# Optimization experiments

Measured on AMD Instinct MI355X. Metric: run time of the kernel, lower is better.

The kernel has to match this reference:

```python
import jax, jax.numpy as jnp
import numpy as np

N_HEAD = 16

def setup_inputs() -> dict:
    key = jax.random.key(0)
    ks = jax.random.split(key, 5)
    B, T, C = 8, 1024, 1024
    s = 0.02
    return {
        "x": jax.random.normal(ks[0], (B, T, C), jnp.float32),
        "W_qkv": jax.random.normal(ks[1], (C, 3 * C), jnp.float32) * s,
        "b_qkv": jnp.zeros((3 * C,), jnp.float32),
        "W_proj": jax.random.normal(ks[2], (C, C), jnp.float32) * s,
        "b_proj": jnp.zeros((C,), jnp.float32),
    }

def reference(x, W_qkv, b_qkv, W_proj, b_proj):
    B, T, C = x.shape
    H = N_HEAD
    hs = C // H
    qkv = x @ W_qkv + b_qkv                       # [B,T,3C]
    q, k, v = jnp.split(qkv, 3, axis=-1)
    # [B,T,C] -> [B,H,T,hs]
    q = q.reshape(B, T, H, hs).transpose(0, 2, 1, 3)
    k = k.reshape(B, T, H, hs).transpose(0, 2, 1, 3)
    v = v.reshape(B, T, H, hs).transpose(0, 2, 1, 3)
    scores = jnp.einsum('bhqd,bhkd->bhqk', q, k) * (hs ** -0.5)  # [B,H,T,T]
    causal = jnp.tril(jnp.ones((T, T), dtype=bool))
    scores = jnp.where(causal[None, None], scores, jnp.finfo(scores.dtype).min)
    attn = jax.nn.softmax(scores, axis=-1)
    # dropout layers are identity in eval mode
    out = jnp.einsum('bhqk,bhkd->bhqd', attn, v)  # [B,H,T,hs]
    out = out.transpose(0, 2, 1, 3).reshape(B, T, C)
    return out @ W_proj + b_proj
```

## Files before the change

kernel.cpp:

```cpp
#include <hip/hip_runtime.h>

#define TT 1024
#define CC 1024
#define NH 16
#define HS 64

typedef __attribute__((ext_vector_type(8))) short short8;
typedef __attribute__((ext_vector_type(4))) float f32x4;

__device__ inline unsigned short f2bf(float f) {
  unsigned int u = __float_as_uint(f);
  unsigned int r = u + 0x7FFFu + ((u >> 16) & 1u);
  return (unsigned short)(r >> 16);
}

__device__ inline unsigned int cvtpk_bf16(float lo, float hi) {
  unsigned int r;
  asm("v_cvt_pk_bf16_f32 %0, %1, %2" : "=v"(r) : "v"(lo), "v"(hi));
  return r;
}

#define GLDS16(g, l)                                                         \
  __builtin_amdgcn_global_load_lds(                                          \
      (const __attribute__((address_space(1))) void*)(g),                    \
      (__attribute__((address_space(3))) void*)(l), 16, 0, 0)

__global__ __launch_bounds__(256) void f32_to_bf16(
    const float* __restrict__ in, unsigned short* __restrict__ out, int n4) {
  int i = (blockIdx.x * 256 + threadIdx.x);
  if (i >= n4) return;
  float4 v = *(const float4*)&in[(size_t)i * 4];
  ushort4 o;
  o.x = f2bf(v.x); o.y = f2bf(v.y); o.z = f2bf(v.z); o.w = f2bf(v.w);
  *(ushort4*)&out[(size_t)i * 4] = o;
}

__global__ __launch_bounds__(256) void transpose_to_bf16(
    const float* __restrict__ W, unsigned short* __restrict__ Wt,
    int K, int N) {
  __shared__ float tile[32][33];
  const int n0 = blockIdx.x * 32, k0 = blockIdx.y * 32;
  const int t = threadIdx.x;
  {
    const int kr = t >> 3;
    const int nc = (t & 7) * 4;
    float4 v = *(const float4*)&W[(size_t)(k0 + kr) * N + n0 + nc];
    tile[kr][nc + 0] = v.x; tile[kr][nc + 1] = v.y;
    tile[kr][nc + 2] = v.z; tile[kr][nc + 3] = v.w;
  }
  __syncthreads();
  {
    const int nr = t >> 3;
    const int kc = (t & 7) * 4;
    ushort4 o;
    o.x = f2bf(tile[kc + 0][nr]);
    o.y = f2bf(tile[kc + 1][nr]);
    o.z = f2bf(tile[kc + 2][nr]);
    o.w = f2bf(tile[kc + 3][nr]);
    *(ushort4*)&Wt[(size_t)(n0 + nr) * K + k0 + kc] = o;
  }
}

template <bool BF16_OUT>
__global__ __launch_bounds__(512, 2) void gemm_8ph(
    const unsigned short* __restrict__ A,
    const unsigned short* __restrict__ Bt,
    const float* __restrict__ bias,
    void* __restrict__ Cv,
    int M, int N, int K) {
  extern __shared__ __attribute__((aligned(16))) unsigned short smg[];
  typedef __attribute__((address_space(3))) unsigned short lds_us;
  lds_us* sml = (lds_us*)smg;

  const int tid = threadIdx.x;
  const int w = tid >> 6, l = tid & 63;
  const int lr = l & 15, lg = l >> 4;
  const int wm = w >> 2, wn = w & 3;

  const int gx = gridDim.x;
  const int nwg = gx * gridDim.y;
  int f = blockIdx.y * gx + blockIdx.x;
  f = (f & 7) * (nwg >> 3) + (f >> 3);
  const int bx = f % gx, by = f / gx;
  const int brow = by * 256, bcol = bx * 256;

  const int r0 = w * 8 + (l >> 3);
  const int cs = (l & 7) ^ (l >> 3);
  const unsigned short* Asrc = A + (size_t)(brow + r0) * K + cs * 8;
  const unsigned short* Bsrc = Bt + (size_t)(bcol + r0) * K + cs * 8;
  const int wlds = w * 512;

#define ST_A(dd, hh, qq, kt)                                                 \
  GLDS16(Asrc + (size_t)((hh)*128 + (qq)*64) * K + (kt) * 64,                \
         sml + (dd)*16384 + (hh)*8192 + (qq)*4096 + wlds)
#define ST_B(dd, hh, qq, kt)                                                 \
  GLDS16(Bsrc + (size_t)((hh)*128 + (qq)*64) * K + (kt) * 64,                \
         sml + 32768 + (dd)*16384 + (hh)*8192 + (qq)*4096 + wlds)

  f32x4 acc[8][4] = {};
  short8 afA[4][2], bfB[4][2];

  const int ck0 = ((lg) ^ (lr & 7)) * 8;
  const int ck1 = ((4 | lg) ^ (lr & 7)) * 8;
  const int abase = wm * 8192 + lr * 64;
  const int bbase = 32768 + (wn >> 1) * 8192 + (wn & 1) * 4096 + lr * 64;

#define LDA(MI0)                                                             \
  _Pragma("unroll") for (int mi = 0; mi < 4; ++mi) {                         \
    afA[mi][0] = *(const short8*)(smg + bb * 16384 + abase + ((MI0) + mi) * 1024 + ck0); \
    afA[mi][1] = *(const short8*)(smg + bb * 16384 + abase + ((MI0) + mi) * 1024 + ck1); \
  }
#define LDB(NI0)                                                             \
  _Pragma("unroll") for (int ni = 0; ni < 2; ++ni) {                         \
    bfB[(NI0) + ni][0] = *(const short8*)(smg + bb * 16384 + bbase + ((NI0) + ni) * 1024 + ck0); \
    bfB[(NI0) + ni][1] = *(const short8*)(smg + bb * 16384 + bbase + ((NI0) + ni) * 1024 + ck1); \
  }
#define MFMA_Q(MI0, NI0)                                                     \
  __builtin_amdgcn_s_setprio(1);                                             \
  _Pragma("unroll") for (int mi = 0; mi < 4; ++mi)                           \
  _Pragma("unroll") for (int ni = 0; ni < 2; ++ni)                           \
  _Pragma("unroll") for (int ks = 0; ks < 2; ++ks)                           \
    acc[(MI0) + mi][(NI0) + ni] = __builtin_amdgcn_mfma_f32_16x16x32_bf16(   \
        afA[mi][ks], bfB[(NI0) + ni][ks], acc[(MI0) + mi][(NI0) + ni], 0, 0, 0); \
  __builtin_amdgcn_s_setprio(0);
#define WAIT_LGKM                                                            \
  asm volatile("s_waitcnt lgkmcnt(0)" ::: "memory");                         \
  __builtin_amdgcn_sched_barrier(0);

  const int nk = K >> 6;

#pragma unroll
  for (int tt = 0; tt < 2; ++tt) {
    ST_A(tt, 0, 0, tt); ST_A(tt, 0, 1, tt); ST_A(tt, 1, 0, tt); ST_A(tt, 1, 1, tt);
    ST_B(tt, 0, 0, tt); ST_B(tt, 0, 1, tt); ST_B(tt, 1, 0, tt); ST_B(tt, 1, 1, tt);
  }

  for (int t = 0; t < nk; ++t) {
    const int bb = t & 1;
    const bool dostage = (t + 2 < nk);
    if (t == nk - 1) { asm volatile("s_waitcnt vmcnt(0)" ::: "memory"); }
    else             { asm volatile("s_waitcnt vmcnt(8)" ::: "memory"); }
    __builtin_amdgcn_sched_barrier(0);
    __builtin_amdgcn_s_barrier();
    LDA(0); LDB(0);
    WAIT_LGKM;
    MFMA_Q(0, 0);
    __builtin_amdgcn_s_barrier();
    LDB(2);
    WAIT_LGKM;
    MFMA_Q(0, 2);
    __builtin_amdgcn_s_barrier();
    if (dostage) { ST_B(bb, 0, 0, t + 2); ST_B(bb, 0, 1, t + 2);
                   ST_B(bb, 1, 0, t + 2); ST_B(bb, 1, 1, t + 2); }
    LDA(4);
    WAIT_LGKM;
    MFMA_Q(4, 0);
    __builtin_amdgcn_s_barrier();
    if (dostage) { ST_A(bb, 0, 0, t + 2); ST_A(bb, 0, 1, t + 2);
                   ST_A(bb, 1, 0, t + 2); ST_A(bb, 1, 1, t + 2); }
    MFMA_Q(4, 2);
    __builtin_amdgcn_s_barrier();
  }
#undef ST_A
#undef ST_B
#undef LDA
#undef LDB
#undef MFMA_Q
#undef WAIT_LGKM

#pragma unroll
  for (int ni = 0; ni < 4; ++ni) {
    const int col = bcol + wn * 64 + ni * 16 + lr;
    const float bv = bias[col];
#pragma unroll
    for (int mi = 0; mi < 8; ++mi) {
      const int row0 = brow + wm * 128 + mi * 16 + lg * 4;
#pragma unroll
      for (int j = 0; j < 4; ++j) {
        const float val = acc[mi][ni][j] + bv;
        if (BF16_OUT)
          ((unsigned short*)Cv)[(size_t)(row0 + j) * N + col] = f2bf(val);
        else
          ((float*)Cv)[(size_t)(row0 + j) * N + col] = val;
      }
    }
  }
}

template <bool BF16_OUT>
__global__ __launch_bounds__(512, 4) void gemm_bt_256(
    const unsigned short* __restrict__ A,
    const unsigned short* __restrict__ Bt,
    const float* __restrict__ bias,
    void* __restrict__ Cv,
    int M, int N, int K) {
  __shared__ __attribute__((aligned(16))) unsigned short As[2][256 * 32];
  __shared__ __attribute__((aligned(16))) unsigned short Bs[2][128 * 32];

  const int tid = threadIdx.x;
  const int w = tid >> 6, l = tid & 63;
  const int lr = l & 15, lg = l >> 4;
  const int wr = w >> 1, wc = w & 1;

  const int gx = gridDim.x;
  const int nwg = gx * gridDim.y;
  int f = blockIdx.y * gx + blockIdx.x;
  f = (f & 7) * (nwg >> 3) + (f >> 3);
  const int bx = f % gx, by = f / gx;
  const int brow = by * 256, bcol = bx * 128;

  const int ga0 = tid, ga1 = 512 + tid;
  const int ar0 = ga0 >> 2, ac0 = ga0 & 3;
  const int ar1 = ga1 >> 2, ac1 = ga1 & 3;
  const int br_ = tid >> 2, bc_ = tid & 3;
  const unsigned short* Asrc0 =
      A + (size_t)(brow + ar0) * K + (ac0 ^ ((ar0 >> 1) & 3)) * 8;
  const unsigned short* Asrc1 =
      A + (size_t)(brow + ar1) * K + (ac1 ^ ((ar1 >> 1) & 3)) * 8;
  const unsigned short* Bsrc =
      Bt + (size_t)(bcol + br_) * K + (bc_ ^ ((br_ >> 1) & 3)) * 8;

  typedef __attribute__((address_space(3))) unsigned short lds_us;

#define STAGE(bb, kt)                                                        \
  do {                                                                       \
    const int k0_ = (kt) * 32;                                               \
    GLDS16(Asrc0 + k0_, (lds_us*)&As[bb][0] + ga0 * 8);                      \
    GLDS16(Asrc1 + k0_, (lds_us*)&As[bb][0] + ga1 * 8);                      \
    GLDS16(Bsrc + k0_, (lds_us*)&Bs[bb][0] + tid * 8);                       \
  } while (0)

  f32x4 acc[4][4] = {};

  const int sfr = ((((lr >> 1) & 3) ^ lg) * 8);
  const int arow0 = wr * 64 + lr;
  const int brow0 = wc * 64 + lr;

#define KSTEP(cur, kt, VMASM, DOSTAGE)                                       \
  do {                                                                       \
    asm volatile(VMASM ::: "memory");                                        \
    __builtin_amdgcn_sched_barrier(0);                                       \
    __builtin_amdgcn_s_barrier();                                            \
    short8 af[4], bf[4];                                                     \
    _Pragma("unroll") for (int mi_ = 0; mi_ < 4; ++mi_)                      \
        af[mi_] = *(const short8*)&As[cur][(arow0 + mi_ * 16) * 32 + sfr];   \
    _Pragma("unroll") for (int ni_ = 0; ni_ < 4; ++ni_)                      \
        bf[ni_] = *(const short8*)&Bs[cur][(brow0 + ni_ * 16) * 32 + sfr];   \
    asm volatile("s_waitcnt lgkmcnt(0)" ::: "memory");                       \
    __builtin_amdgcn_sched_barrier(0);                                       \
    __builtin_amdgcn_s_barrier();                                            \
    __builtin_amdgcn_sched_barrier(0);                                       \
    if (DOSTAGE) STAGE(cur, (kt) + 2);                                       \
    __builtin_amdgcn_s_setprio(1);                                           \
    _Pragma("unroll") for (int mi_ = 0; mi_ < 4; ++mi_)                      \
        _Pragma("unroll") for (int ni_ = 0; ni_ < 4; ++ni_)                  \
            acc[mi_][ni_] = __builtin_amdgcn_mfma_f32_16x16x32_bf16(         \
                af[mi_], bf[ni_], acc[mi_][ni_], 0, 0, 0);                   \
    __builtin_amdgcn_s_setprio(0);                                           \
  } while (0)

  const int nk = K >> 5;
  STAGE(0, 0);
  STAGE(1, 1);
  int cur = 0;
  for (int t = 0; t < nk - 1; ++t) {
    KSTEP(cur, t, "s_waitcnt vmcnt(3)", (t + 2 < nk));
    cur ^= 1;
  }
  KSTEP(cur, nk - 1, "s_waitcnt vmcnt(0)", false);
#undef KSTEP
#undef STAGE

#pragma unroll
  for (int ni = 0; ni < 4; ++ni) {
    const int col = bcol + wc * 64 + ni * 16 + lr;
    const float bv = bias[col];
#pragma unroll
    for (int mi = 0; mi < 4; ++mi) {
      const int row0 = brow + wr * 64 + mi * 16 + lg * 4;
#pragma unroll
      for (int j = 0; j < 4; ++j) {
        const float val = acc[mi][ni][j] + bv;
        if (BF16_OUT)
          ((unsigned short*)Cv)[(size_t)(row0 + j) * N + col] = f2bf(val);
        else
          ((float*)Cv)[(size_t)(row0 + j) * N + col] = val;
      }
    }
  }
}

#define C1 0.18033688f

__global__ __launch_bounds__(256) void attn_mfma(
    const unsigned short* __restrict__ qkv, unsigned short* __restrict__ aout) {
  const int bh = blockIdx.y;
  const int b = bh >> 4, h = bh & 15;
  const int tid = threadIdx.x;
  const int w = tid >> 6;
  const int l = tid & 63;
  const int lr = l & 15;
  const int lg = l >> 4;

  __shared__ __attribute__((aligned(16))) unsigned short Kl[64 * 64];
  __shared__ __attribute__((aligned(16))) unsigned short Vt[64 * 64];
  __shared__ __attribute__((aligned(16))) unsigned short Pq[4][32 * 64];

  const size_t row3c = 3 * CC;
  const unsigned short* qbase = qkv + (size_t)(b * TT) * row3c + h * HS;
  const unsigned short* kbase = qbase + CC;
  const unsigned short* vbase = qbase + 2 * CC;

  const int ksrow = 16 * w + (l >> 3);
  const int ksbyte = (((l & 7) ^ (l >> 3)) << 4);
  typedef __attribute__((address_space(3))) unsigned short lds_us;
  lds_us* KlW0 = (lds_us*)Kl + (16 * w) * 64;
  lds_us* KlW1 = (lds_us*)Kl + (16 * w + 8) * 64;

#pragma unroll 1
  for (int pass = 0; pass < 2; ++pass) {
    const int qt = pass ? (7 - blockIdx.x) : blockIdx.x;
    const int qw = qt * 128 + w * 32;

    short8 aq[2][2];
#pragma unroll
    for (int mi = 0; mi < 2; ++mi)
#pragma unroll
      for (int ks = 0; ks < 2; ++ks)
        aq[mi][ks] = *(const short8*)(qbase +
            (size_t)(qw + mi * 16 + lr) * row3c + ks * 32 + lg * 8);

    f32x4 sOT[4][2] = {};
    float lpart[2] = {0.f, 0.f};

    const int ntiles = 2 * qt + 2;
    for (int kt = 0; kt < ntiles; ++kt) {
      const int k0 = kt * 64;
      GLDS16((const char*)(kbase + (size_t)(k0 + ksrow) * row3c) + ksbyte, KlW0);
      GLDS16((const char*)(kbase + (size_t)(k0 + 8 + ksrow) * row3c) + ksbyte, KlW1);
      {
        const unsigned short* vsrc = vbase + (size_t)(k0 + l) * row3c + 16 * w;
        short8 v0 = *(const short8*)(vsrc);
        short8 v1 = *(const short8*)(vsrc + 8);
#pragma unroll
        for (int i = 0; i < 8; ++i) {
          const int d0 = 16 * w + i, d1 = d0 + 8;
          Vt[(d0 * 64 + l) ^ ((d0 & 7) << 3)] = (unsigned short)v0[i];
          Vt[(d1 * 64 + l) ^ ((d1 & 7) << 3)] = (unsigned short)v1[i];
        }
      }
      __syncthreads();

      if (k0 <= qw + 31) {
        f32x4 sacc[4][2] = {};
        short8 ak[4][2];
#pragma unroll
        for (int ni = 0; ni < 4; ++ni) {
          const int tok = ni * 16 + lr;
          const int sw = (tok & 7) << 3;
#pragma unroll
          for (int ks = 0; ks < 2; ++ks)
            ak[ni][ks] = *(const short8*)&Kl[tok * 64 + ((ks * 32 + lg * 8) ^ sw)];
        }
#pragma unroll
        for (int ni = 0; ni < 4; ++ni)
#pragma unroll
          for (int mi = 0; mi < 2; ++mi)
#pragma unroll
            for (int ks = 0; ks < 2; ++ks)
              sacc[ni][mi] = __builtin_amdgcn_mfma_f32_16x16x32_bf16(
                  ak[ni][ks], aq[mi][ks], sacc[ni][mi], 0, 0, 0);

        const bool diag = (k0 + 63 > qw);
#pragma unroll
        for (int mi = 0; mi < 2; ++mi) {
          const int qloc = mi * 16 + lr;
          const int qglob = qw + qloc;
          const int psw = (qloc & 7) << 3;
          float ls = 0.f;
#pragma unroll
          for (int ni = 0; ni < 4; ++ni) {
            float p[4];
#pragma unroll
            for (int jj = 0; jj < 4; ++jj) {
              const float pv = exp2f(fmaf(sacc[ni][mi][jj], C1, -2.0f));
              const int kvg = k0 + ni * 16 + lg * 4 + jj;
              p[jj] = (diag && (kvg > qglob)) ? 0.f : pv;
            }
            ls += (p[0] + p[1]) + (p[2] + p[3]);
            uint2 pk;
            pk.x = cvtpk_bf16(p[0], p[1]);
            pk.y = cvtpk_bf16(p[2], p[3]);
            *(uint2*)&Pq[w][qloc * 64 + ((ni * 16 + lg * 4) ^ psw)] = pk;
          }
          lpart[mi] += ls;
        }

        short8 av[4][2], bp[2][2];
#pragma unroll
        for (int nd = 0; nd < 4; ++nd) {
          const int d = nd * 16 + lr;
          const int sw = (d & 7) << 3;
#pragma unroll
          for (int ks = 0; ks < 2; ++ks)
            av[nd][ks] = *(const short8*)&Vt[d * 64 + ((ks * 32 + lg * 8) ^ sw)];
        }
#pragma unroll
        for (int mi = 0; mi < 2; ++mi) {
          const int qloc = mi * 16 + lr;
          const int psw = (qloc & 7) << 3;
#pragma unroll
          for (int ks = 0; ks < 2; ++ks)
            bp[mi][ks] = *(const short8*)&Pq[w][qloc * 64 + ((ks * 32 + lg * 8) ^ psw)];
        }
#pragma unroll
        for (int nd = 0; nd < 4; ++nd)
#pragma unroll
          for (int mi = 0; mi < 2; ++mi)
#pragma unroll
            for (int ks = 0; ks < 2; ++ks)
              sOT[nd][mi] = __builtin_amdgcn_mfma_f32_16x16x32_bf16(
                  av[nd][ks], bp[mi][ks], sOT[nd][mi], 0, 0, 0);
      }
      __syncthreads();
    }

#pragma unroll
    for (int mi = 0; mi < 2; ++mi) {
      float ls = lpart[mi];
      ls += __shfl_xor(ls, 16);
      ls += __shfl_xor(ls, 32);
      const float inv = 1.f / ls;
      const size_t row = (size_t)(b * TT + qw + mi * 16 + lr);
#pragma unroll
      for (int nd = 0; nd < 4; ++nd) {
        uint2 pk;
        pk.x = cvtpk_bf16(sOT[nd][mi][0] * inv, sOT[nd][mi][1] * inv);
        pk.y = cvtpk_bf16(sOT[nd][mi][2] * inv, sOT[nd][mi][3] * inv);
        *(uint2*)&aout[row * CC + h * HS + nd * 16 + lg * 4] = pk;
      }
    }
  }
}

extern "C" void kernel_launch(void* const* d_in, const int* in_sizes, int n_in,
                              void* d_out, int out_size, void* d_ws, size_t ws_size,
                              hipStream_t stream) {
  const float* x     = (const float*)d_in[0];
  const float* Wqkv  = (const float*)d_in[1];
  const float* bqkv  = (const float*)d_in[2];
  const float* Wproj = (const float*)d_in[3];
  const float* bproj = (const float*)d_in[4];
  float* out = (float*)d_out;

  char* ws = (char*)d_ws;
  unsigned short* qkvb   = (unsigned short*)ws;
  unsigned short* xb     = (unsigned short*)(ws + 50331648);
  unsigned short* attnb  = (unsigned short*)(ws + 67108864);
  unsigned short* wqkvt  = (unsigned short*)(ws + 83886080);
  unsigned short* wprojt = (unsigned short*)(ws + 90177536);

  const int M = 8 * TT;

  (void)hipFuncSetAttribute((const void*)&gemm_8ph<true>,
      hipFuncAttributeMaxDynamicSharedMemorySize, 131072);

  f32_to_bf16<<<dim3(8192), dim3(256), 0, stream>>>(x, xb, M * CC / 4);
  transpose_to_bf16<<<dim3(96, 32), dim3(256), 0, stream>>>(Wqkv, wqkvt, CC, 3 * CC);
  transpose_to_bf16<<<dim3(32, 32), dim3(256), 0, stream>>>(Wproj, wprojt, CC, CC);

  gemm_8ph<true><<<dim3(3 * CC / 256, M / 256), dim3(512), 131072, stream>>>(
      xb, wqkvt, bqkv, qkvb, M, 3 * CC, CC);

  attn_mfma<<<dim3(4, 8 * NH), dim3(256), 0, stream>>>(qkvb, attnb);

  gemm_bt_256<false><<<dim3(CC / 128, M / 256), dim3(512), 0, stream>>>(
      attnb, wprojt, bproj, out, M, CC, CC);
}
```

Baseline: 251.7 us.

## Restagger A/B global-to-LDS prefetch across GEMM k-loop phases

Reworks the double-buffered GEMM main loop so A tiles for step t+1 and B tiles for step t+2 are issued in smaller pieces, interleaved between the four MFMA quarters, rather than in two bursts. The vmcnt wait moves to the end of each iteration and extra barriers are added around each staging point. The aim is to spread global_load_lds traffic more evenly so it overlaps with MFMA work. The cost is more barriers per iteration, and a tighter one-step lookahead for A that could expose load latency.

```diff
diff --git a/kernel.cpp b/kernel.cpp
--- a/kernel.cpp
+++ b/kernel.cpp
@@ -123,49 +123,54 @@
     acc[(MI0) + mi][(NI0) + ni] = __builtin_amdgcn_mfma_f32_16x16x32_bf16(   \
         afA[mi][ks], bfB[(NI0) + ni][ks], acc[(MI0) + mi][(NI0) + ni], 0, 0, 0); \
   __builtin_amdgcn_s_setprio(0);
+#define PIN __builtin_amdgcn_sched_barrier(0)
+#define BAR __builtin_amdgcn_s_barrier()
 #define WAIT_LGKM                                                            \
   asm volatile("s_waitcnt lgkmcnt(0)" ::: "memory");                         \
   __builtin_amdgcn_sched_barrier(0);
 
   const int nk = K >> 6;
 
-#pragma unroll
-  for (int tt = 0; tt < 2; ++tt) {
-    ST_A(tt, 0, 0, tt); ST_A(tt, 0, 1, tt); ST_A(tt, 1, 0, tt); ST_A(tt, 1, 1, tt);
-    ST_B(tt, 0, 0, tt); ST_B(tt, 0, 1, tt); ST_B(tt, 1, 0, tt); ST_B(tt, 1, 1, tt);
-  }
+  ST_B(0, 0, 0, 0); ST_B(0, 0, 1, 0); ST_B(0, 1, 0, 0); ST_B(0, 1, 1, 0);
+  ST_A(0, 0, 0, 0); ST_A(0, 0, 1, 0); ST_A(0, 1, 0, 0); ST_A(0, 1, 1, 0);
+  ST_B(1, 0, 0, 1); ST_B(1, 0, 1, 1); ST_B(1, 1, 0, 1); ST_B(1, 1, 1, 1);
+  asm volatile("s_waitcnt vmcnt(4)" ::: "memory");
+  PIN; BAR;
 
   for (int t = 0; t < nk; ++t) {
-    const int bb = t & 1;
-    const bool dostage = (t + 2 < nk);
-    if (t == nk - 1) { asm volatile("s_waitcnt vmcnt(0)" ::: "memory"); }
-    else             { asm volatile("s_waitcnt vmcnt(8)" ::: "memory"); }
-    __builtin_amdgcn_sched_barrier(0);
-    __builtin_amdgcn_s_barrier();
+    const int bb = t & 1, nb = bb ^ 1;
     LDA(0); LDB(0);
+    if (t + 1 < nk) { ST_A(nb, 0, 0, t + 1); ST_A(nb, 0, 1, t + 1); }
+    PIN; BAR;
     WAIT_LGKM;
     MFMA_Q(0, 0);
-    __builtin_amdgcn_s_barrier();
+    BAR;
     LDB(2);
+    if (t + 1 < nk) { ST_A(nb, 1, 0, t + 1); ST_A(nb, 1, 1, t + 1); }
+    PIN; BAR;
     WAIT_LGKM;
     MFMA_Q(0, 2);
-    __builtin_amdgcn_s_barrier();
-    if (dostage) { ST_B(bb, 0, 0, t + 2); ST_B(bb, 0, 1, t + 2);
-                   ST_B(bb, 1, 0, t + 2); ST_B(bb, 1, 1, t + 2); }
+    BAR;
     LDA(4);
+    if (t + 2 < nk) { ST_B(bb, 0, 0, t + 2); ST_B(bb, 0, 1, t + 2); }
+    PIN; BAR;
     WAIT_LGKM;
     MFMA_Q(4, 0);
-    __builtin_amdgcn_s_barrier();
-    if (dostage) { ST_A(bb, 0, 0, t + 2); ST_A(bb, 0, 1, t + 2);
-                   ST_A(bb, 1, 0, t + 2); ST_A(bb, 1, 1, t + 2); }
+    BAR;
+    if (t + 2 < nk) { ST_B(bb, 1, 0, t + 2); ST_B(bb, 1, 1, t + 2); }
+    PIN; BAR;
     MFMA_Q(4, 2);
-    __builtin_amdgcn_s_barrier();
+    if (t + 2 < nk)      { asm volatile("s_waitcnt vmcnt(4)" ::: "memory"); PIN; }
+    else if (t + 1 < nk) { asm volatile("s_waitcnt vmcnt(0)" ::: "memory"); PIN; }
+    BAR;
   }
 #undef ST_A
 #undef ST_B
 #undef LDA
 #undef LDB
 #undef MFMA_Q
+#undef PIN
+#undef BAR
 #undef WAIT_LGKM
 
 #pragma unroll
```

Result: no change. 256.2 us (+1.8%).
